# Kernel optimization log

Measured on AMD Instinct MI355X. Metric: run time of the kernel, lower is better.

The kernel has to match this reference:

```python
import jax, jax.numpy as jnp
import numpy as np

NUM_LAYER = 5
EMB = 300
N_NODES = 100000
N_EDGES = 250000
BN_EPS = 1e-5


def setup_inputs() -> dict:
    key = jax.random.key(0)
    ks = jax.random.split(key, 12)
    s = 0.05
    inp = {
        "x": jax.random.randint(ks[0], (N_NODES, 2), 0, 3),
        "edge_index": jax.random.randint(ks[1], (2, N_EDGES), 0, N_NODES),
        "edge_attr": jax.random.randint(ks[2], (N_EDGES, 2), 0, 3),
        # node-feature embedding tables
        "x_emb1": jax.random.normal(ks[3], (120, EMB), jnp.float32) * s,
        "x_emb2": jax.random.normal(ks[4], (3, EMB), jnp.float32) * s,
        # per-layer edge embedding tables (bond type=6, bond direction=3)
        "e_emb1": jax.random.normal(ks[5], (NUM_LAYER, 6, EMB), jnp.float32) * s,
        "e_emb2": jax.random.normal(ks[6], (NUM_LAYER, 3, EMB), jnp.float32) * s,
        # per-layer GIN MLP: Linear(D,2D) -> ReLU -> Linear(2D,D); weights stored (out,in)
        "w1": jax.random.normal(ks[7], (NUM_LAYER, 2 * EMB, EMB), jnp.float32) * s,
        "b1": jnp.zeros((NUM_LAYER, 2 * EMB), jnp.float32),
        "w2": jax.random.normal(ks[8], (NUM_LAYER, EMB, 2 * EMB), jnp.float32) * s,
        "b2": jnp.zeros((NUM_LAYER, EMB), jnp.float32),
        # per-layer BatchNorm1d affine params (training-mode batch stats)
        "gamma": jnp.ones((NUM_LAYER, EMB), jnp.float32),
        "beta": jnp.zeros((NUM_LAYER, EMB), jnp.float32),
    }
    return inp


def reference(x, edge_index, edge_attr, x_emb1, x_emb2, e_emb1, e_emb2, w1, b1, w2, b2, gamma, beta):
    n = x.shape[0]
    # input node embedding: atom type + chirality tag
    h = x_emb1[x[:, 0]] + x_emb2[x[:, 1]]  # [N, D]

    # add self loops (self-loop edge_attr = [4, 0])
    loop = jnp.arange(n, dtype=edge_index.dtype)
    src = jnp.concatenate([edge_index[0], loop])  # [E+N]
    dst = jnp.concatenate([edge_index[1], loop])
    ea0 = jnp.concatenate([edge_attr[:, 0], jnp.full((n,), 4, edge_attr.dtype)])
    ea1 = jnp.concatenate([edge_attr[:, 1], jnp.zeros((n,), edge_attr.dtype)])

    for l in range(NUM_LAYER):
        e = e_emb1[l][ea0] + e_emb2[l][ea1]           # [E+N, D] edge embeddings
        msg = h[src] + e                               # gather + message
        agg = jax.ops.segment_sum(msg, dst, num_segments=n)  # scatter-add aggregate
        hid = jnp.maximum(agg @ w1[l].T + b1[l], 0.0)  # GIN MLP
        h2 = hid @ w2[l].T + b2[l]
        # BatchNorm1d (training-mode batch statistics, biased variance)
        mu = h2.mean(axis=0)
        var = jnp.mean((h2 - mu) ** 2, axis=0)
        h2 = (h2 - mu) * jax.lax.rsqrt(var + BN_EPS) * gamma[l] + beta[l]
        if l < NUM_LAYER - 1:
            h2 = jnp.maximum(h2, 0.0)  # ReLU (dropout ratio = 0)
        h = h2

    # JK == 'last'
    return h
```

## Files before the change

### kernel.cpp

```cpp
#include <hip/hip_runtime.h>
#include <hip/hip_bf16.h>

#define DD 300
#define C4 75
#define AGS 320
#define BN_EPS 1e-5f

typedef _Float16 f16x8 __attribute__((ext_vector_type(8)));
typedef float f32x4 __attribute__((ext_vector_type(4)));

union PackH4 { _Float16 h[4]; uint2 u; };

__device__ __forceinline__ void gld_lds16(const void* g, void* lds) {
    __builtin_amdgcn_global_load_lds(
        (const __attribute__((address_space(1))) void*)g,
        (__attribute__((address_space(3))) void*)lds, 16, 0, 0);
}

__global__ __launch_bounds__(256) void embed_kernel(
    const int* __restrict__ x, const float* __restrict__ emb1,
    const float* __restrict__ emb2, float* __restrict__ h, int hs, int total4)
{
    int i = blockIdx.x * 256 + threadIdx.x;
    if (i >= total4) return;
    int node = i / C4, chunk = i - node * C4;
    int a = x[2 * node], b = x[2 * node + 1];
    int c = chunk << 2;
    float4 v1 = *(const float4*)(emb1 + (size_t)a * DD + c);
    float4 v2 = *(const float4*)(emb2 + (size_t)b * DD + c);
    float4 r;
    r.x = v1.x + v2.x; r.y = v1.y + v2.y; r.z = v1.z + v2.z; r.w = v1.w + v2.w;
    *(float4*)(h + (size_t)node * hs + c) = r;
}

__global__ __launch_bounds__(256) void build_ec_kernel(
    const float* __restrict__ e1, const float* __restrict__ e2, float* __restrict__ ec)
{
    int gid = blockIdx.x * 256 + threadIdx.x;
    if (gid >= 5 * 18 * DD) return;
    int l = gid / (18 * DD);
    int rem = gid - l * 18 * DD;
    int combo = rem / DD;
    int c = rem - combo * DD;
    int a0 = combo / 3, a1 = combo - a0 * 3;
    ec[gid] = e1[(size_t)l * 6 * DD + a0 * DD + c] + e2[(size_t)l * 3 * DD + a1 * DD + c];
}

__global__ __launch_bounds__(256) void deg_kernel(
    const int* __restrict__ ei, int* __restrict__ deg, int E)
{
    int e = blockIdx.x * 256 + threadIdx.x;
    if (e >= E) return;
    atomicAdd(&deg[ei[E + e]], 1);
}

__global__ __launch_bounds__(256) void scan1_kernel(
    const int* __restrict__ deg, int* __restrict__ pre, int* __restrict__ blockSum, int n)
{
    __shared__ int sa[256], sb[256];
    int t = threadIdx.x;
    int base = blockIdx.x * 1024 + t * 4;
    int v0 = (base + 0 < n) ? deg[base + 0] : 0;
    int v1 = (base + 1 < n) ? deg[base + 1] : 0;
    int v2 = (base + 2 < n) ? deg[base + 2] : 0;
    int v3 = (base + 3 < n) ? deg[base + 3] : 0;
    int tot = v0 + v1 + v2 + v3;
    sa[t] = tot;
    __syncthreads();
    int* src = sa; int* dst = sb;
    for (int off = 1; off < 256; off <<= 1) {
        int v = src[t];
        if (t >= off) v += src[t - off];
        dst[t] = v;
        __syncthreads();
        int* tmp = src; src = dst; dst = tmp;
    }
    int incl = src[t];
    int excl = incl - tot;
    if (base + 0 < n) pre[base + 0] = excl;
    if (base + 1 < n) pre[base + 1] = excl + v0;
    if (base + 2 < n) pre[base + 2] = excl + v0 + v1;
    if (base + 3 < n) pre[base + 3] = excl + v0 + v1 + v2;
    if (t == 255) blockSum[blockIdx.x] = incl;
}

__global__ __launch_bounds__(256) void scan2_kernel(int* __restrict__ blockSum, int nb)
{
    __shared__ int sa[256], sb[256];
    int t = threadIdx.x;
    int v = (t < nb) ? blockSum[t] : 0;
    sa[t] = v;
    __syncthreads();
    int* src = sa; int* dst = sb;
    for (int off = 1; off < 256; off <<= 1) {
        int x = src[t];
        if (t >= off) x += src[t - off];
        dst[t] = x;
        __syncthreads();
        int* tmp = src; src = dst; dst = tmp;
    }
    if (t < nb) blockSum[t] = src[t] - v;
}

__global__ __launch_bounds__(256) void scan3_kernel(
    const int* __restrict__ pre, const int* __restrict__ blockSum,
    int* __restrict__ rowPtr, int* __restrict__ cursor, int n, int E)
{
    int idx = blockIdx.x * 256 + threadIdx.x;
    if (idx > n) return;
    int v = (idx < n) ? pre[idx] + blockSum[idx >> 10] : E;
    rowPtr[idx] = v;
    if (idx < n) cursor[idx] = v;
}

__global__ __launch_bounds__(256) void fill_kernel(
    const int* __restrict__ ei, const int* __restrict__ ea,
    int* __restrict__ cursor, int* __restrict__ edges, int E)
{
    int e = blockIdx.x * 256 + threadIdx.x;
    if (e >= E) return;
    int src = ei[e];
    int dst = ei[E + e];
    int combo = ea[2 * e] * 3 + ea[2 * e + 1];
    int slot = atomicAdd(&cursor[dst], 1);
    edges[slot] = src | (combo << 18);
}

__global__ __launch_bounds__(256) void gather_kernel(
    const float* __restrict__ h, int hs, const int* __restrict__ rowPtr,
    const int* __restrict__ edges, const float* __restrict__ ec,
    const float* __restrict__ scale, const float* __restrict__ shift, int use_affine,
    _Float16* __restrict__ agg, int n)
{
    int gid = blockIdx.x * 256 + threadIdx.x;
    int node = gid / C4, ch = gid - node * C4;
    if (node >= n) return;
    int c = ch << 2;
    float4 sc, sh;
    if (use_affine) {
        sc = *(const float4*)(scale + c);
        sh = *(const float4*)(shift + c);
    }
    float4 acc = *(const float4*)(h + (size_t)node * hs + c);
    if (use_affine) {
        acc.x = fmaxf(fmaf(sc.x, acc.x, sh.x), 0.f);
        acc.y = fmaxf(fmaf(sc.y, acc.y, sh.y), 0.f);
        acc.z = fmaxf(fmaf(sc.z, acc.z, sh.z), 0.f);
        acc.w = fmaxf(fmaf(sc.w, acc.w, sh.w), 0.f);
    }
    float4 es = *(const float4*)(ec + 12 * DD + c);
    acc.x += es.x; acc.y += es.y; acc.z += es.z; acc.w += es.w;

    int start = rowPtr[node], end = rowPtr[node + 1];
    for (int e = start; e < end; ++e) {
        int pk = edges[e];
        int src = pk & 0x3FFFF;
        int combo = pk >> 18;
        float4 hv = *(const float4*)(h + (size_t)src * hs + c);
        if (use_affine) {
            hv.x = fmaxf(fmaf(sc.x, hv.x, sh.x), 0.f);
            hv.y = fmaxf(fmaf(sc.y, hv.y, sh.y), 0.f);
            hv.z = fmaxf(fmaf(sc.z, hv.z, sh.z), 0.f);
            hv.w = fmaxf(fmaf(sc.w, hv.w, sh.w), 0.f);
        }
        float4 ev = *(const float4*)(ec + combo * DD + c);
        acc.x += hv.x + ev.x;
        acc.y += hv.y + ev.y;
        acc.z += hv.z + ev.z;
        acc.w += hv.w + ev.w;
    }
    PackH4 p;
    p.h[0] = (_Float16)acc.x;
    p.h[1] = (_Float16)acc.y;
    p.h[2] = (_Float16)acc.z;
    p.h[3] = (_Float16)acc.w;
    *(uint2*)(agg + (size_t)node * AGS + c) = p.u;
}

__global__ __launch_bounds__(256) void convert_w_kernel(
    const float* __restrict__ w, _Float16* __restrict__ wf,
    int rows, int cols, int rowsP, int colsP)
{
    int gid = blockIdx.x * 256 + threadIdx.x;
    int total = 5 * rowsP * colsP;
    if (gid >= total) return;
    int l = gid / (rowsP * colsP);
    int rem = gid - l * (rowsP * colsP);
    int r = rem / colsP;
    int k = rem - r * colsP;
    float v = (r < rows && k < cols) ? w[((size_t)l * rows + r) * cols + k] : 0.f;
    wf[gid] = (_Float16)v;
}

template <bool OUT_F16, bool DO_STATS>
__global__ __launch_bounds__(512, 2) void mfma_gemm_lds(
    const _Float16* __restrict__ A, const _Float16* __restrict__ W,
    const float* __restrict__ bias,
    _Float16* __restrict__ outH, float* __restrict__ outF,
    float* __restrict__ sum, float* __restrict__ sumsq,
    int M, int Kp, int outStride, int outN, int nCol)
{
    __shared__ __attribute__((aligned(16))) unsigned short sA[2][128 * 64];
    __shared__ __attribute__((aligned(16))) unsigned short sB[2][128 * 64];

    const int bid = blockIdx.x;
    const int group = bid / (8 * nCol);
    const int within = bid - group * 8 * nCol;
    const int rowT = group * 8 + (within & 7);
    const int colT = within >> 3;
    const int bm = rowT << 7;
    const int bn = colT << 7;

    const int tid = threadIdx.x;
    const int lane = tid & 63, wv = tid >> 6;
    const int wy = wv & 3, wx = wv >> 2;
    const int quad = lane >> 4, l16 = lane & 15;

    const int r8 = lane >> 3;
    const int chv = (lane & 7) ^ r8;

    f32x4 acc[2][4] = {};

    auto STAGE = [&](int buf, int k0) {
#pragma unroll
        for (int j = 0; j < 2; ++j) {
            int rloc = wv * 16 + j * 8 + r8;
            gld_lds16(A + (size_t)(bm + rloc) * Kp + k0 + chv * 8,
                      &sA[buf][(wv * 16 + j * 8) * 64]);
        }
#pragma unroll
        for (int j = 0; j < 2; ++j) {
            int rloc = wv * 16 + j * 8 + r8;
            gld_lds16(W + (size_t)(bn + rloc) * Kp + k0 + chv * 8,
                      &sB[buf][(wv * 16 + j * 8) * 64]);
        }
    };

    auto COMPUTE = [&](int buf) {
#pragma unroll
        for (int kk = 0; kk < 2; ++kk) {
            f16x8 a[2], b[4];
#pragma unroll
            for (int i = 0; i < 2; ++i) {
                int rA = wy * 32 + i * 16 + l16;
                int slotA = (kk * 4 + quad) ^ (rA & 7);
                a[i] = *(const f16x8*)&sA[buf][rA * 64 + slotA * 8];
            }
#pragma unroll
            for (int j = 0; j < 4; ++j) {
                int rB = wx * 64 + j * 16 + l16;
                int slotB = (kk * 4 + quad) ^ (rB & 7);
                b[j] = *(const f16x8*)&sB[buf][rB * 64 + slotB * 8];
            }
#pragma unroll
            for (int i = 0; i < 2; ++i)
#pragma unroll
                for (int j = 0; j < 4; ++j)
                    acc[i][j] = __builtin_amdgcn_mfma_f32_16x16x32_f16(
                        a[i], b[j], acc[i][j], 0, 0, 0);
        }
    };

    const int nT = Kp >> 6;
    STAGE(0, 0);
    for (int t = 0; t < nT; ++t) {
        if (t + 1 < nT) {
            STAGE((t + 1) & 1, (t + 1) << 6);
            asm volatile("s_waitcnt vmcnt(4)" ::: "memory");
        } else {
            asm volatile("s_waitcnt vmcnt(0)" ::: "memory");
        }
        __builtin_amdgcn_s_barrier();
        __builtin_amdgcn_sched_barrier(0);
        COMPUTE(t & 1);
        __builtin_amdgcn_s_barrier();
        __builtin_amdgcn_sched_barrier(0);
    }

#pragma unroll
    for (int j = 0; j < 4; ++j) {
        int col = bn + wx * 64 + j * 16 + l16;
        float bv = (col < outN) ? bias[col] : 0.f;
        float cs = 0.f, cq = 0.f;
#pragma unroll
        for (int i = 0; i < 2; ++i) {
            int rowBase = bm + wy * 32 + i * 16 + (quad << 2);
#pragma unroll
            for (int r = 0; r < 4; ++r) {
                int row = rowBase + r;
                if (row >= M) continue;
                float v = acc[i][j][r] + bv;
                if constexpr (DO_STATS) { if (col < outN) { cs += v; cq += v * v; } }
                if constexpr (OUT_F16) {
                    float o = (col < outN) ? fmaxf(v, 0.f) : 0.f;
                    outH[(size_t)row * outStride + col] = (_Float16)o;
                } else {
                    if (col < outStride) outF[(size_t)row * outStride + col] = v;
                }
            }
        }
        if constexpr (DO_STATS) {
            cs += __shfl_down(cs, 32); cq += __shfl_down(cq, 32);
            cs += __shfl_down(cs, 16); cq += __shfl_down(cq, 16);
            if (quad == 0 && col < outN) {
                atomicAdd(&sum[col], cs);
                atomicAdd(&sumsq[col], cq);
            }
        }
    }
}

__global__ void finalize_kernel(
    const float* __restrict__ sum, const float* __restrict__ sumsq,
    const float* __restrict__ gamma, const float* __restrict__ beta,
    float* __restrict__ scale, float* __restrict__ shift, float inv_n)
{
    int c = threadIdx.x;
    if (c < DD) {
        float mu = sum[c] * inv_n;
        float var = sumsq[c] * inv_n - mu * mu;
        float inv = rsqrtf(var + BN_EPS);
        float sc = gamma[c] * inv;
        scale[c] = sc;
        shift[c] = fmaf(-mu, sc, beta[c]);
    }
}

__global__ __launch_bounds__(256) void apply_kernel(
    const float* __restrict__ h, int hs, const float* __restrict__ scale,
    const float* __restrict__ shift, float* __restrict__ out, int total4)
{
    int i = blockIdx.x * 256 + threadIdx.x;
    if (i >= total4) return;
    int node = i / C4;
    int c = (i - node * C4) << 2;
    float4 v = *(const float4*)(h + (size_t)node * hs + c);
    float4 r;
    r.x = fmaf(scale[c + 0], v.x, shift[c + 0]);
    r.y = fmaf(scale[c + 1], v.y, shift[c + 1]);
    r.z = fmaf(scale[c + 2], v.z, shift[c + 2]);
    r.w = fmaf(scale[c + 3], v.w, shift[c + 3]);
    ((float4*)out)[i] = r;
}

extern "C" void kernel_launch(void* const* d_in, const int* in_sizes, int n_in,
                              void* d_out, int out_size, void* d_ws, size_t ws_size,
                              hipStream_t stream)
{
    const int*   x      = (const int*)d_in[0];
    const int*   ei     = (const int*)d_in[1];
    const int*   ea     = (const int*)d_in[2];
    const float* x_emb1 = (const float*)d_in[3];
    const float* x_emb2 = (const float*)d_in[4];
    const float* e_emb1 = (const float*)d_in[5];
    const float* e_emb2 = (const float*)d_in[6];
    const float* w1     = (const float*)d_in[7];
    const float* b1     = (const float*)d_in[8];
    const float* w2     = (const float*)d_in[9];
    const float* b2     = (const float*)d_in[10];
    const float* gamma  = (const float*)d_in[11];
    const float* beta   = (const float*)d_in[12];

    const int n = in_sizes[0] / 2;
    const int E = in_sizes[1] / 2;
    const int nRowT = (n + 127) / 128;
    const int nRowTP = ((nRowT + 7) / 8) * 8;
    const int MpA = nRowTP * 128;
    const int Kp1 = AGS, Kp2 = 640;
    const int NP1 = 640, NP2 = 384;

    char* p = (char*)d_ws;
    auto alloc = [&](size_t bytes) -> void* {
        void* r = (void*)p;
        p += (bytes + 255) & ~(size_t)255;
        return r;
    };
    _Float16* agg  = (_Float16*)alloc((size_t)MpA * Kp1 * 2);
    _Float16* hid  = (_Float16*)alloc((size_t)MpA * Kp2 * 2);
    _Float16* w1f  = (_Float16*)alloc((size_t)5 * NP1 * Kp1 * 2);
    _Float16* w2f  = (_Float16*)alloc((size_t)5 * NP2 * Kp2 * 2);
    float* ec     = (float*)alloc((size_t)5 * 18 * DD * 4);
    int*   deg    = (int*)alloc((size_t)n * 4);
    int*   rowPtr = (int*)alloc((size_t)(n + 1) * 4);
    int*   cursor = (int*)alloc((size_t)n * 4);
    int*   blockSum = (int*)alloc(256 * 4);
    int*   edges  = (int*)alloc((size_t)E * 4);
    float* sum   = (float*)alloc(320 * 4);
    float* sumsq = (float*)alloc(320 * 4);
    float* scale = (float*)alloc(320 * 4);
    float* shift = (float*)alloc(320 * 4);

    const size_t used = (size_t)(p - (char*)d_ws);
    const size_t hBytes = (size_t)n * 320 * 4;
    float* h;
    int HS;
    if (ws_size >= used + hBytes) {
        h = (float*)alloc(hBytes);
        HS = 320;
    } else {
        h = (float*)d_out;
        HS = DD;
    }

    const int total4 = n * C4;
    const int nb = (n + 1023) / 1024;

    {
        convert_w_kernel<<<(5 * NP1 * Kp1 + 255) / 256, 256, 0, stream>>>(w1, w1f, 600, 300, NP1, Kp1);
        convert_w_kernel<<<(5 * NP2 * Kp2 + 255) / 256, 256, 0, stream>>>(w2, w2f, 300, 600, NP2, Kp2);
        build_ec_kernel<<<(5 * 18 * DD + 255) / 256, 256, 0, stream>>>(e_emb1, e_emb2, ec);
        hipMemsetAsync(deg, 0, (size_t)n * 4, stream);
        deg_kernel<<<(E + 255) / 256, 256, 0, stream>>>(ei, deg, E);
        scan1_kernel<<<nb, 256, 0, stream>>>(deg, cursor , blockSum, n);
        scan2_kernel<<<1, 256, 0, stream>>>(blockSum, nb);
        scan3_kernel<<<(n + 256) / 256, 256, 0, stream>>>(cursor, blockSum, rowPtr, deg , n, E);
        fill_kernel<<<(E + 255) / 256, 256, 0, stream>>>(ei, ea, deg, edges, E);
        hipMemsetAsync(agg, 0, (size_t)MpA * Kp1 * 2, stream);
        embed_kernel<<<(total4 + 255) / 256, 256, 0, stream>>>(x, x_emb1, x_emb2, h, HS, total4);
    }

    const int gatherTotal = n * C4;
    const int nCol1 = NP1 / 128;
    const int nCol2 = NP2 / 128;
    const int g1 = nRowTP * nCol1;
    const int g2 = nRowTP * nCol2;

    for (int l = 0; l < 5; l++) {
        hipMemsetAsync(sum, 0, 2 * 320 * sizeof(float), stream);
        gather_kernel<<<(gatherTotal + 255) / 256, 256, 0, stream>>>(
            h, HS, rowPtr, edges, ec + (size_t)l * 18 * DD, scale, shift, l > 0 ? 1 : 0,
            agg, n);
        mfma_gemm_lds<true, false><<<g1, 512, 0, stream>>>(
            agg, w1f + (size_t)l * NP1 * Kp1,
            b1 + (size_t)l * 600, hid, nullptr, nullptr, nullptr,
            n, Kp1, Kp2, 600, nCol1);
        mfma_gemm_lds<false, true><<<g2, 512, 0, stream>>>(
            hid, w2f + (size_t)l * NP2 * Kp2,
            b2 + (size_t)l * 300, nullptr, h, sum, sumsq,
            n, Kp2, HS, 300, nCol2);
        finalize_kernel<<<1, 320, 0, stream>>>(sum, sumsq, gamma + (size_t)l * DD,
                                               beta + (size_t)l * DD, scale, shift,
                                               1.0f / (float)n);
    }
    apply_kernel<<<(total4 + 255) / 256, 256, 0, stream>>>(h, HS, scale, shift,
                                                           (float*)d_out, total4);
}
```

Measured before the change: 1.879 ms.

## Load GEMM A operand directly into registers, stage only B via LDS

The GEMM now reads A fragments straight from global memory into registers, prefetching the next k-tile, and keeps only the weight tile staged in LDS through a double buffer. The K-loop trip count becomes a template parameter so the loop fully unrolls, and launch bounds ask for 4 blocks per CU instead of 2. This halves LDS use and drops the LDS round trip for A. In exchange, A is loaded redundantly by the two wx waves, the global accesses are less coalesced, and register pressure rises under the tighter occupancy target.

New measurement: 2.221 ms. +18.2%, slower.

```diff
diff --git a/kernel.cpp b/kernel.cpp
--- a/kernel.cpp
+++ b/kernel.cpp
@@ -192,15 +192,14 @@
     wf[gid] = (_Float16)v;
 }
 
-template <bool OUT_F16, bool DO_STATS>
-__global__ __launch_bounds__(512, 2) void mfma_gemm_lds(
+template <int NT, bool OUT_F16, bool DO_STATS>
+__global__ __launch_bounds__(512, 4) void mfma_gemm(
     const _Float16* __restrict__ A, const _Float16* __restrict__ W,
     const float* __restrict__ bias,
     _Float16* __restrict__ outH, float* __restrict__ outF,
     float* __restrict__ sum, float* __restrict__ sumsq,
     int M, int Kp, int outStride, int outN, int nCol)
 {
-    __shared__ __attribute__((aligned(16))) unsigned short sA[2][128 * 64];
     __shared__ __attribute__((aligned(16))) unsigned short sB[2][128 * 64];
 
     const int bid = blockIdx.x;
@@ -221,13 +220,9 @@
 
     f32x4 acc[2][4] = {};
 
-    auto STAGE = [&](int buf, int k0) {
-#pragma unroll
-        for (int j = 0; j < 2; ++j) {
-            int rloc = wv * 16 + j * 8 + r8;
-            gld_lds16(A + (size_t)(bm + rloc) * Kp + k0 + chv * 8,
-                      &sA[buf][(wv * 16 + j * 8) * 64]);
-        }
+    const _Float16* aBase = A + (size_t)(bm + wy * 32 + l16) * Kp + quad * 8;
+
+    auto STAGEB = [&](int buf, int k0) {
 #pragma unroll
         for (int j = 0; j < 2; ++j) {
             int rloc = wv * 16 + j * 8 + r8;
@@ -236,45 +231,54 @@
         }
     };
 
-    auto COMPUTE = [&](int buf) {
+    auto LOADA = [&](f16x8 (&dst)[2][2], int k0) {
+#pragma unroll
+        for (int i = 0; i < 2; ++i)
+#pragma unroll
+            for (int kk = 0; kk < 2; ++kk)
+                dst[i][kk] = *(const f16x8*)(aBase + (size_t)i * 16 * Kp + k0 + kk * 32);
+    };
+
+    f16x8 aCur[2][2], aNxt[2][2];
+    STAGEB(0, 0);
+    LOADA(aCur, 0);
+
+#pragma unroll
+    for (int t = 0; t < NT; ++t) {
+        if (t + 1 < NT) {
+            STAGEB((t + 1) & 1, (t + 1) << 6);
+            LOADA(aNxt, (t + 1) << 6);
+            asm volatile("s_waitcnt vmcnt(6)" ::: "memory");
+        } else {
+            asm volatile("s_waitcnt vmcnt(0)" ::: "memory");
+        }
+        __builtin_amdgcn_s_barrier();
+        __builtin_amdgcn_sched_barrier(0);
 #pragma unroll
         for (int kk = 0; kk < 2; ++kk) {
-            f16x8 a[2], b[4];
-#pragma unroll
-            for (int i = 0; i < 2; ++i) {
-                int rA = wy * 32 + i * 16 + l16;
-                int slotA = (kk * 4 + quad) ^ (rA & 7);
-                a[i] = *(const f16x8*)&sA[buf][rA * 64 + slotA * 8];
-            }
+            f16x8 b[4];
 #pragma unroll
             for (int j = 0; j < 4; ++j) {
                 int rB = wx * 64 + j * 16 + l16;
                 int slotB = (kk * 4 + quad) ^ (rB & 7);
-                b[j] = *(const f16x8*)&sB[buf][rB * 64 + slotB * 8];
+                b[j] = *(const f16x8*)&sB[t & 1][rB * 64 + slotB * 8];
             }
 #pragma unroll
             for (int i = 0; i < 2; ++i)
 #pragma unroll
                 for (int j = 0; j < 4; ++j)
                     acc[i][j] = __builtin_amdgcn_mfma_f32_16x16x32_f16(
-                        a[i], b[j], acc[i][j], 0, 0, 0);
-        }
-    };
-
-    const int nT = Kp >> 6;
-    STAGE(0, 0);
-    for (int t = 0; t < nT; ++t) {
-        if (t + 1 < nT) {
-            STAGE((t + 1) & 1, (t + 1) << 6);
-            asm volatile("s_waitcnt vmcnt(4)" ::: "memory");
-        } else {
-            asm volatile("s_waitcnt vmcnt(0)" ::: "memory");
+                        aCur[i][kk], b[j], acc[i][j], 0, 0, 0);
         }
         __builtin_amdgcn_s_barrier();
         __builtin_amdgcn_sched_barrier(0);
-        COMPUTE(t & 1);
-        __builtin_amdgcn_s_barrier();
-        __builtin_amdgcn_sched_barrier(0);
+        if (t + 1 < NT) {
+#pragma unroll
+            for (int i = 0; i < 2; ++i)
+#pragma unroll
+                for (int kk = 0; kk < 2; ++kk)
+                    aCur[i][kk] = aNxt[i][kk];
+        }
     }
 
 #pragma unroll
@@ -430,11 +434,11 @@
         gather_kernel<<<(gatherTotal + 255) / 256, 256, 0, stream>>>(
             h, HS, rowPtr, edges, ec + (size_t)l * 18 * DD, scale, shift, l > 0 ? 1 : 0,
             agg, n);
-        mfma_gemm_lds<true, false><<<g1, 512, 0, stream>>>(
+        mfma_gemm<5, true, false><<<g1, 512, 0, stream>>>(
             agg, w1f + (size_t)l * NP1 * Kp1,
             b1 + (size_t)l * 600, hid, nullptr, nullptr, nullptr,
             n, Kp1, Kp2, 600, nCol1);
-        mfma_gemm_lds<false, true><<<g2, 512, 0, stream>>>(
+        mfma_gemm<10, false, true><<<g2, 512, 0, stream>>>(
             hid, w2f + (size_t)l * NP2 * Kp2,
             b2 + (size_t)l * 300, nullptr, h, sum, sumsq,
             n, Kp2, HS, 300, nCol2);
```
